# Kernel tuning notes

Measured on AMD Instinct MI355X. Metric: run time of the kernel, lower is better.

## Reference

```python
import jax, jax.numpy as jnp
import numpy as np

VOCAB = 50000
DIM = 512
NUM_NUM = 1000  # ids [0, 1000) are '<num>i</num>' tokens with value i


def setup_inputs() -> dict:
    key = jax.random.key(0)
    k1, k2 = jax.random.split(key)
    x = jax.random.randint(k1, (8, 4096), 0, VOCAB, dtype=jnp.int32)
    # learned embedding, init normal(0, 0.1) as in the torch module
    weight = jax.random.normal(k2, (VOCAB, DIM), dtype=jnp.float32) * 0.1
    ids = jnp.arange(VOCAB)
    is_num = ids < NUM_NUM
    num_value = jnp.where(is_num, ids, 0).astype(jnp.int32)  # numeric value of '<num>v</num>'
    return {"x": x, "weight": weight, "num_value": num_value, "is_num": is_num}


def reference(x, weight, num_value, is_num):
    dim = weight.shape[1]
    # sinusoidal row for numeric tokens: sin((v/1000) * (i+1)), i in [0, dim)
    freqs = jnp.arange(1, dim + 1, dtype=jnp.float32)                 # (D,)
    scaled = num_value.astype(jnp.float32) / 1000.0                   # (V,)
    sin_table = jnp.sin(scaled[:, None] * freqs[None, :])             # (V, D)
    # merged static table: sinusoidal where numeric, learned otherwise
    table = jnp.where(is_num[:, None], sin_table, weight)             # (V, D)
    return table[x]                                                   # (B, S, D)
```

## Files before the change

### kernel.cpp

```cpp
#include <hip/hip_runtime.h>


#define DIM 512
#define NUM_NUM 1000
#define GRID_BLOCKS 2048

typedef float floatx4 __attribute__((ext_vector_type(4)));

__global__ __launch_bounds__(256) void CustomEmbedding_kernel(
    const int* __restrict__ x,
    const float* __restrict__ weight,
    float* __restrict__ out,
    long long total)
{
    long long stride = (long long)gridDim.x * 256;
    for (long long i = blockIdx.x * 256LL + threadIdx.x; i < total; i += stride) {
        int tok = (int)(i >> 7);
        int d   = ((int)i & 127) << 2;

        int idx = x[tok];
        floatx4 v;
        if (idx < NUM_NUM) {
            float base = (float)idx * 1e-3f;
            v.x = sinf(base * (float)(d + 1));
            v.y = sinf(base * (float)(d + 2));
            v.z = sinf(base * (float)(d + 3));
            v.w = sinf(base * (float)(d + 4));
        } else {
            v = *reinterpret_cast<const floatx4*>(weight + (size_t)idx * DIM + d);
        }
        __builtin_nontemporal_store(v, reinterpret_cast<floatx4*>(out + (i << 2)));
    }
}

extern "C" void kernel_launch(void* const* d_in, const int* in_sizes, int n_in,
                              void* d_out, int out_size, void* d_ws, size_t ws_size,
                              hipStream_t stream) {
    const int*   x      = (const int*)d_in[0];
    const float* weight = (const float*)d_in[1];
    float* out = (float*)d_out;

    int n_tok = in_sizes[0];
    long long total = (long long)n_tok * 128;
    long long need  = (total + 255) / 256;
    int grid = (int)(need < GRID_BLOCKS ? need : GRID_BLOCKS);
    CustomEmbedding_kernel<<<grid, 256, 0, stream>>>(x, weight, out, total);
}
```

Measured before the change: 25.24 us.

## Assign whole tokens per wavefront and load two rows unconditionally before sin

Each wavefront now handles whole embedding rows, two tokens per iteration, with each lane moving two float4 chunks per row. All four weight loads are issued up front, even for numeric tokens whose values are then overwritten by sin, so more memory requests are in flight per thread and the per-element index arithmetic goes away. The cost is wasted weight reads for numeric tokens (rows below 1000 exist, so this is safe) and higher register pressure.

```diff
diff --git a/kernel.cpp b/kernel.cpp
--- a/kernel.cpp
+++ b/kernel.cpp
@@ -11,25 +11,52 @@
     const int* __restrict__ x,
     const float* __restrict__ weight,
     float* __restrict__ out,
-    long long total)
+    int n_tok)
 {
-    long long stride = (long long)gridDim.x * 256;
-    for (long long i = blockIdx.x * 256LL + threadIdx.x; i < total; i += stride) {
-        int tok = (int)(i >> 7);
-        int d   = ((int)i & 127) << 2;
+    int lane    = threadIdx.x & 63;
+    int wave_g  = (blockIdx.x * 256 + threadIdx.x) >> 6;
+    int n_waves = (gridDim.x * 256) >> 6;
 
-        int idx = x[tok];
-        floatx4 v;
-        if (idx < NUM_NUM) {
-            float base = (float)idx * 1e-3f;
-            v.x = sinf(base * (float)(d + 1));
-            v.y = sinf(base * (float)(d + 2));
-            v.z = sinf(base * (float)(d + 3));
-            v.w = sinf(base * (float)(d + 4));
-        } else {
-            v = *reinterpret_cast<const floatx4*>(weight + (size_t)idx * DIM + d);
+    int dA = lane << 2;
+    int dB = 256 + dA;
+
+    for (int t0 = wave_g; t0 < n_tok; t0 += 2 * n_waves) {
+        int t1 = t0 + n_waves;
+        bool has1 = (t1 < n_tok);
+
+        int idx0 = x[t0];
+        int idx1 = has1 ? x[t1] : 0;
+
+        const floatx4* r0 = reinterpret_cast<const floatx4*>(weight + (size_t)idx0 * DIM);
+        const floatx4* r1 = reinterpret_cast<const floatx4*>(weight + (size_t)idx1 * DIM);
+        floatx4 a0 = r0[lane];
+        floatx4 b0 = r0[64 + lane];
+        floatx4 a1 = r1[lane];
+        floatx4 b1 = r1[64 + lane];
+
+        if (idx0 < NUM_NUM) {
+            float base = (float)idx0 * 1e-3f;
+            a0.x = sinf(base * (float)(dA + 1)); a0.y = sinf(base * (float)(dA + 2));
+            a0.z = sinf(base * (float)(dA + 3)); a0.w = sinf(base * (float)(dA + 4));
+            b0.x = sinf(base * (float)(dB + 1)); b0.y = sinf(base * (float)(dB + 2));
+            b0.z = sinf(base * (float)(dB + 3)); b0.w = sinf(base * (float)(dB + 4));
         }
-        __builtin_nontemporal_store(v, reinterpret_cast<floatx4*>(out + (i << 2)));
+        if (has1 && idx1 < NUM_NUM) {
+            float base = (float)idx1 * 1e-3f;
+            a1.x = sinf(base * (float)(dA + 1)); a1.y = sinf(base * (float)(dA + 2));
+            a1.z = sinf(base * (float)(dA + 3)); a1.w = sinf(base * (float)(dA + 4));
+            b1.x = sinf(base * (float)(dB + 1)); b1.y = sinf(base * (float)(dB + 2));
+            b1.z = sinf(base * (float)(dB + 3)); b1.w = sinf(base * (float)(dB + 4));
+        }
+
+        floatx4* o0 = reinterpret_cast<floatx4*>(out + (size_t)t0 * DIM);
+        __builtin_nontemporal_store(a0, o0 + lane);
+        __builtin_nontemporal_store(b0, o0 + 64 + lane);
+        if (has1) {
+            floatx4* o1 = reinterpret_cast<floatx4*>(out + (size_t)t1 * DIM);
+            __builtin_nontemporal_store(a1, o1 + lane);
+            __builtin_nontemporal_store(b1, o1 + 64 + lane);
+        }
     }
 }
 
@@ -41,8 +68,5 @@
     float* out = (float*)d_out;
 
     int n_tok = in_sizes[0];
-    long long total = (long long)n_tok * 128;
-    long long need  = (total + 255) / 256;
-    int grid = (int)(need < GRID_BLOCKS ? need : GRID_BLOCKS);
-    CustomEmbedding_kernel<<<grid, 256, 0, stream>>>(x, weight, out, total);
+    CustomEmbedding_kernel<<<GRID_BLOCKS, 256, 0, stream>>>(x, weight, out, n_tok);
 }
```

Result: slower. 26.38 us (+4.5%).
